# Kernel tuning notes

Hardware: AMD Instinct MI355X
Metric: run time of the kernel (lower is better)

## Reference

```python
import jax, jax.numpy as jnp
import numpy as np

HEADS = 8
DIM_HEAD = 64
SCALE = DIM_HEAD ** -0.5


def setup_inputs() -> dict:
    key = jax.random.key(0)
    ks = jax.random.split(key, 7)
    B, Nq, Nc = 4, 2048, 2048
    Dq, Dc = 1024, 768
    inner = HEADS * DIM_HEAD  # 512
    x = jax.random.normal(ks[0], (B, Nq, Dq), dtype=jnp.float32)
    context = jax.random.normal(ks[1], (B, Nc, Dc), dtype=jnp.float32)
    # Linear weights stored as (in, out) so y = x @ W, matching torch Linear math.
    Wq = jax.random.normal(ks[2], (Dq, inner), dtype=jnp.float32) * (Dq ** -0.5)
    Wk = jax.random.normal(ks[3], (Dc, inner), dtype=jnp.float32) * (Dc ** -0.5)
    Wv = jax.random.normal(ks[4], (Dc, inner), dtype=jnp.float32) * (Dc ** -0.5)
    Wo = jax.random.normal(ks[5], (inner, Dq), dtype=jnp.float32) * (inner ** -0.5)
    bo = jax.random.normal(ks[6], (Dq,), dtype=jnp.float32) * 0.01
    return {"x": x, "context": context, "Wq": Wq, "Wk": Wk, "Wv": Wv, "Wo": Wo, "bo": bo}


def reference(x, context, Wq, Wk, Wv, Wo, bo):
    B, Nq, _ = x.shape
    # projections -> [b, n, h, d]
    q = (x @ Wq).reshape(B, Nq, HEADS, DIM_HEAD)
    k = (context @ Wk).reshape(B, context.shape[1], HEADS, DIM_HEAD)
    v = (context @ Wv).reshape(B, context.shape[1], HEADS, DIM_HEAD)
    # scores [b, h, i, j]
    sim = jnp.einsum('bihd,bjhd->bhij', q, k) * SCALE
    attn = jax.nn.softmax(sim, axis=-1)
    out = jnp.einsum('bhij,bjhd->bihd', attn, v)  # [b, i, h, d]
    out = out.reshape(B, Nq, HEADS * DIM_HEAD)
    return out @ Wo + bo
```

## Files before the change

kernel.cpp:

```cpp
#include <hip/hip_runtime.h>
#include <hip/hip_bf16.h>


typedef __bf16 bf16_8 __attribute__((ext_vector_type(8)));
typedef __bf16 bf16_4 __attribute__((ext_vector_type(4)));
typedef float f32_4 __attribute__((ext_vector_type(4)));

#define AS1 __attribute__((address_space(1)))
#define AS3 __attribute__((address_space(3)))

__device__ __forceinline__ void gld_lds16(const __bf16* g, __bf16* l) {
  __builtin_amdgcn_global_load_lds((AS1 unsigned int*)(void*)g,
                                   (AS3 unsigned int*)(void*)l, 16, 0, 0);
}

__device__ __forceinline__ void lds_fence() {
  __asm__ volatile("" ::: "memory");
  __builtin_amdgcn_s_waitcnt(0xC07F);
  __asm__ volatile("" ::: "memory");
}

__global__ __launch_bounds__(256) void prep(
    const float* __restrict__ x, const float* __restrict__ ctx,
    const float* __restrict__ Wq, const float* __restrict__ Wk,
    const float* __restrict__ Wv, const float* __restrict__ Wo,
    __bf16* __restrict__ xb, __bf16* __restrict__ ctxb,
    __bf16* __restrict__ WqT, __bf16* __restrict__ WkT,
    __bf16* __restrict__ WvT, __bf16* __restrict__ WoT) {
  int tb = blockIdx.x;
  if (tb >= 1792) {
    tb -= 1792;
    const float* src;
    __bf16* dst;
    size_t base;
    if (tb < 4096) { src = x; dst = xb; base = (size_t)tb * 2048; }
    else { src = ctx; dst = ctxb; base = (size_t)(tb - 4096) * 2048; }
    const size_t idx = base + threadIdx.x * 8;
    const f32_4 f0 = *(const f32_4*)(src + idx);
    const f32_4 f1 = *(const f32_4*)(src + idx + 4);
    bf16_8 v;
#pragma unroll
    for (int i = 0; i < 4; ++i) { v[i] = (__bf16)f0[i]; v[4 + i] = (__bf16)f1[i]; }
    *(bf16_8*)(dst + idx) = v;
    return;
  }
  __shared__ __bf16 t[32][33];
  const float* W; __bf16* Wt; int K, N;
  if (tb < 512)       { W = Wq; Wt = WqT; K = 1024; N = 512; }
  else if (tb < 896)  { tb -= 512;  W = Wk; Wt = WkT; K = 768; N = 512; }
  else if (tb < 1280) { tb -= 896;  W = Wv; Wt = WvT; K = 768; N = 512; }
  else                { tb -= 1280; W = Wo; Wt = WoT; K = 512; N = 1024; }
  const int nx = N >> 5;
  const int n0 = (tb % nx) * 32, k0 = (tb / nx) * 32;
  const int tx = threadIdx.x & 31, ty = threadIdx.x >> 5;
#pragma unroll
  for (int r = 0; r < 32; r += 8)
    t[ty + r][tx] = (__bf16)W[(size_t)(k0 + ty + r) * N + n0 + tx];
  __syncthreads();
#pragma unroll
  for (int r = 0; r < 32; r += 8)
    Wt[(size_t)(n0 + ty + r) * K + k0 + tx] = t[tx][ty + r];
}

__global__ __launch_bounds__(256, 2) void proj(
    const __bf16* __restrict__ xb, const __bf16* __restrict__ ctxb,
    const __bf16* __restrict__ WqT, const __bf16* __restrict__ WkvT,
    __bf16* __restrict__ Qb, __bf16* __restrict__ Kbuf,
    __bf16* __restrict__ Vtb) {
  __shared__ __align__(16) __bf16 As[2][128 * 64];
  __shared__ __align__(16) __bf16 Bs[2][128 * 64];
  int tb = blockIdx.x;
  const __bf16 *A, *Bt;
  int K, bm, bn, mode;
  if (tb < 256) {
    A = xb; Bt = WqT; K = 1024; mode = 0;
    bn = (tb & 3) << 7; bm = (tb >> 2) << 7;
  } else {
    tb -= 256;
    A = ctxb; Bt = WkvT; K = 768; mode = 1;
    bn = (tb & 7) << 7; bm = (tb >> 3) << 7;
  }
  const int tid = threadIdx.x;
  const int lane = tid & 63;
  const int wave = tid >> 6;
  const int wi = (wave >> 1) * 64;
  const int wn = (wave & 1) * 64;
  const int lrow = lane & 15;
  const int quad = lane >> 4;
  const int lkey = lrow & 7;
  const int srow = tid >> 3;
  const int scol = (tid & 7) * 8;
  const int swz = (((scol >> 3) ^ (srow & 7)) * 8);

  f32_4 acc[4][4];
#pragma unroll
  for (int i = 0; i < 4; ++i)
#pragma unroll
    for (int j = 0; j < 4; ++j)
#pragma unroll
      for (int r = 0; r < 4; ++r) acc[i][j][r] = 0.0f;

  auto stage = [&](int buf, int kt) {
#pragma unroll
    for (int r = 0; r < 4; ++r) {
      const int row = r * 32 + srow;
      gld_lds16(A + (size_t)(bm + row) * K + kt + swz, &As[buf][row * 64 + scol]);
    }
#pragma unroll
    for (int r = 0; r < 4; ++r) {
      const int row = r * 32 + srow;
      gld_lds16(Bt + (size_t)(bn + row) * K + kt + swz, &Bs[buf][row * 64 + scol]);
    }
  };

  stage(0, 0);
  const int nkt = K >> 6;
  for (int kti = 0; kti < nkt; ++kti) {
    __syncthreads();
    if (kti + 1 < nkt) stage((kti + 1) & 1, (kti + 1) * 64);
    const __bf16* Asb = As[kti & 1];
    const __bf16* Bsb = Bs[kti & 1];
#pragma unroll
    for (int ks = 0; ks < 2; ++ks) {
      bf16_8 af[4], bfv[4];
#pragma unroll
      for (int t = 0; t < 4; ++t)
        af[t] = *(const bf16_8*)(Asb + (wi + t * 16 + lrow) * 64 +
                                 (((ks * 4 + quad) ^ lkey) * 8));
#pragma unroll
      for (int t = 0; t < 4; ++t)
        bfv[t] = *(const bf16_8*)(Bsb + (wn + t * 16 + lrow) * 64 +
                                  (((ks * 4 + quad) ^ lkey) * 8));
#pragma unroll
      for (int it = 0; it < 4; ++it)
#pragma unroll
        for (int nt = 0; nt < 4; ++nt)
          acc[it][nt] = __builtin_amdgcn_mfma_f32_16x16x32_bf16(
              af[it], bfv[nt], acc[it][nt], 0, 0, 0);
    }
  }

#pragma unroll
  for (int nt = 0; nt < 4; ++nt) {
    const int c = bn + wn + nt * 16 + lrow;
    if (mode == 0) {
#pragma unroll
      for (int it = 0; it < 4; ++it) {
        const int rbase = bm + wi + it * 16 + quad * 4;
#pragma unroll
        for (int r = 0; r < 4; ++r)
          Qb[(size_t)(rbase + r) * 512 + c] = (__bf16)(acc[it][nt][r] * 0.125f);
      }
    } else if (c < 512) {
#pragma unroll
      for (int it = 0; it < 4; ++it) {
        const int rbase = bm + wi + it * 16 + quad * 4;
#pragma unroll
        for (int r = 0; r < 4; ++r)
          Kbuf[(size_t)(rbase + r) * 512 + c] = (__bf16)acc[it][nt][r];
      }
    } else {
      const int vcol = c - 512;
      const int bhh = ((bm >> 11) << 3) + (vcol >> 6);
      const int d = vcol & 63;
#pragma unroll
      for (int it = 0; it < 4; ++it) {
        const int jb = (bm & 2047) + wi + it * 16 + quad * 4;
        bf16_4 pk;
#pragma unroll
        for (int r = 0; r < 4; ++r) pk[r] = (__bf16)acc[it][nt][r];
        *(bf16_4*)&Vtb[((size_t)(bhh * 64 + d)) * 2048 + jb] = pk;
      }
    }
  }
}

__global__ __launch_bounds__(256, 2) void attn_fwd(const __bf16* __restrict__ Q,
                                                   const __bf16* __restrict__ Kb,
                                                   const __bf16* __restrict__ Vt,
                                                   __bf16* __restrict__ AO) {
  __shared__ __align__(16) __bf16 Ks[2][64 * 64];
  __shared__ __align__(16) __bf16 Vs[2][64 * 64];
  __shared__ __align__(16) __bf16 Pl[4][32 * 64];
  const int tid = threadIdx.x;
  const int lane = tid & 63;
  const int wave = tid >> 6;
  const int bh = blockIdx.y;
  const int b = bh >> 3, h = bh & 7;
  const int i0 = blockIdx.x * 128 + wave * 32;
  const int lrow = lane & 15;
  const int quad = lane >> 4;
  const int lkey = lrow & 7;
  const size_t bq = (size_t)b * 2048;
  const int hc = h * 64;
  __bf16* Pw = &Pl[wave][0];

  const int ssub = lane >> 3;
  const int sch = lane & 7;
  const int sswz = (sch ^ ssub) * 8;

  const __bf16* Kg = Kb + bq * 512 + hc;
  const __bf16* Vg = Vt + (size_t)bh * 64 * 2048;

  auto stage = [&](int buf, int j0) {
#pragma unroll
    for (int t = 0; t < 2; ++t) {
      const int rb = wave * 16 + t * 8;
      gld_lds16(Kg + (size_t)(j0 + rb + ssub) * 512 + sswz, &Ks[buf][rb * 64]);
      gld_lds16(Vg + (size_t)(rb + ssub) * 2048 + j0 + sswz, &Vs[buf][rb * 64]);
    }
  };

  bf16_8 aq[2][2];
#pragma unroll
  for (int it = 0; it < 2; ++it)
#pragma unroll
    for (int ks = 0; ks < 2; ++ks)
      aq[it][ks] = *(const bf16_8*)(Q + (bq + i0 + it * 16 + lrow) * 512 +
                                    hc + ks * 32 + quad * 8);

  float psl[2] = {0.0f, 0.0f};
  f32_4 oacc[2][4];
#pragma unroll
  for (int it = 0; it < 2; ++it)
#pragma unroll
    for (int nt = 0; nt < 4; ++nt)
#pragma unroll
      for (int r = 0; r < 4; ++r) oacc[it][nt][r] = 0.0f;

  stage(0, 0);

  for (int jt = 0; jt < 32; ++jt) {
    __syncthreads();
    if (jt + 1 < 32) stage((jt + 1) & 1, (jt + 1) * 64);
    const __bf16* Ksb = Ks[jt & 1];
    const __bf16* Vsb = Vs[jt & 1];

    f32_4 sacc[2][4];
#pragma unroll
    for (int it = 0; it < 2; ++it)
#pragma unroll
      for (int jn = 0; jn < 4; ++jn)
#pragma unroll
        for (int r = 0; r < 4; ++r) sacc[it][jn][r] = 0.0f;
#pragma unroll
    for (int ks = 0; ks < 2; ++ks) {
      bf16_8 ak[4];
#pragma unroll
      for (int jn = 0; jn < 4; ++jn)
        ak[jn] = *(const bf16_8*)(Ksb + (jn * 16 + lrow) * 64 +
                                  (((ks * 4 + quad) ^ lkey) * 8));
#pragma unroll
      for (int it = 0; it < 2; ++it)
#pragma unroll
        for (int jn = 0; jn < 4; ++jn)
          sacc[it][jn] = __builtin_amdgcn_mfma_f32_16x16x32_bf16(
              ak[jn], aq[it][ks], sacc[it][jn], 0, 0, 0);
    }

#pragma unroll
    for (int it = 0; it < 2; ++it) {
      float ps = 0.0f;
#pragma unroll
      for (int jn = 0; jn < 4; ++jn) {
        bf16_4 pk;
#pragma unroll
        for (int r = 0; r < 4; ++r) {
          const float p = __expf(sacc[it][jn][r]);
          ps += p;
          pk[r] = (__bf16)p;
        }
        *(bf16_4*)(Pw + (it * 16 + lrow) * 64 +
                   (((2 * jn + (quad >> 1)) ^ lkey) * 8) + (quad & 1) * 4) = pk;
      }
      psl[it] += ps;
    }

    lds_fence();

#pragma unroll
    for (int ks2 = 0; ks2 < 2; ++ks2) {
      bf16_8 ap[2], bv[4];
#pragma unroll
      for (int it = 0; it < 2; ++it)
        ap[it] = *(const bf16_8*)(Pw + (it * 16 + lrow) * 64 +
                                  (((ks2 * 4 + quad) ^ lkey) * 8));
#pragma unroll
      for (int nt = 0; nt < 4; ++nt)
        bv[nt] = *(const bf16_8*)(Vsb + (nt * 16 + lrow) * 64 +
                                  (((ks2 * 4 + quad) ^ lkey) * 8));
#pragma unroll
      for (int it = 0; it < 2; ++it)
#pragma unroll
        for (int nt = 0; nt < 4; ++nt)
          oacc[it][nt] = __builtin_amdgcn_mfma_f32_16x16x32_bf16(
              ap[it], bv[nt], oacc[it][nt], 0, 0, 0);
    }
  }

#pragma unroll
  for (int it = 0; it < 2; ++it) {
    float ls = psl[it];
    ls += __shfl_xor(ls, 16);
    ls += __shfl_xor(ls, 32);
    const float inv = 1.0f / ls;
    float ic[4];
#pragma unroll
    for (int r = 0; r < 4; ++r) ic[r] = __shfl(inv, quad * 4 + r);
#pragma unroll
    for (int nt = 0; nt < 4; ++nt)
#pragma unroll
      for (int r = 0; r < 4; ++r) {
        const size_t rg = bq + i0 + it * 16 + quad * 4 + r;
        AO[rg * 512 + hc + nt * 16 + lrow] = (__bf16)(oacc[it][nt][r] * ic[r]);
      }
  }
}

__global__ __launch_bounds__(256, 2) void gemm_out(const __bf16* __restrict__ A,
                                                   const __bf16* __restrict__ Bt,
                                                   float* __restrict__ C,
                                                   const float* __restrict__ bias) {
  __shared__ __align__(16) __bf16 As[2][128 * 64];
  __shared__ __align__(16) __bf16 Bs[2][128 * 64];
  const int K = 512, N = 1024;
  const int tid = threadIdx.x;
  const int lane = tid & 63;
  const int wave = tid >> 6;
  const int wi = (wave >> 1) * 64;
  const int wn = (wave & 1) * 64;
  const int bm = blockIdx.y * 128;
  const int bn = blockIdx.x * 128;
  const int lrow = lane & 15;
  const int quad = lane >> 4;
  const int lkey = lrow & 7;
  const int srow = tid >> 3;
  const int scol = (tid & 7) * 8;
  const int swz = (((scol >> 3) ^ (srow & 7)) * 8);

  f32_4 acc[4][4];
#pragma unroll
  for (int i = 0; i < 4; ++i)
#pragma unroll
    for (int j = 0; j < 4; ++j)
#pragma unroll
      for (int r = 0; r < 4; ++r) acc[i][j][r] = 0.0f;

  auto stage = [&](int buf, int kt) {
#pragma unroll
    for (int r = 0; r < 4; ++r) {
      const int row = r * 32 + srow;
      gld_lds16(A + (size_t)(bm + row) * K + kt + swz, &As[buf][row * 64 + scol]);
      gld_lds16(Bt + (size_t)(bn + row) * K + kt + swz, &Bs[buf][row * 64 + scol]);
    }
  };

  stage(0, 0);
  for (int kti = 0; kti < 8; ++kti) {
    __syncthreads();
    if (kti + 1 < 8) stage((kti + 1) & 1, (kti + 1) * 64);
    const __bf16* Asb = As[kti & 1];
    const __bf16* Bsb = Bs[kti & 1];
#pragma unroll
    for (int ks = 0; ks < 2; ++ks) {
      bf16_8 af[4], bfv[4];
#pragma unroll
      for (int t = 0; t < 4; ++t)
        af[t] = *(const bf16_8*)(Asb + (wi + t * 16 + lrow) * 64 +
                                 (((ks * 4 + quad) ^ lkey) * 8));
#pragma unroll
      for (int t = 0; t < 4; ++t)
        bfv[t] = *(const bf16_8*)(Bsb + (wn + t * 16 + lrow) * 64 +
                                  (((ks * 4 + quad) ^ lkey) * 8));
#pragma unroll
      for (int it = 0; it < 4; ++it)
#pragma unroll
        for (int nt = 0; nt < 4; ++nt)
          acc[it][nt] = __builtin_amdgcn_mfma_f32_16x16x32_bf16(
              af[it], bfv[nt], acc[it][nt], 0, 0, 0);
    }
  }

#pragma unroll
  for (int nt = 0; nt < 4; ++nt) {
    const int c = bn + wn + nt * 16 + lrow;
    const float bv = bias[c];
#pragma unroll
    for (int it = 0; it < 4; ++it) {
      const int rbase = bm + wi + it * 16 + quad * 4;
#pragma unroll
      for (int r = 0; r < 4; ++r)
        C[(size_t)(rbase + r) * N + c] = acc[it][nt][r] + bv;
    }
  }
}

extern "C" void kernel_launch(void* const* d_in, const int* in_sizes, int n_in,
                              void* d_out, int out_size, void* d_ws, size_t ws_size,
                              hipStream_t stream) {
  (void)in_sizes; (void)n_in; (void)out_size; (void)ws_size;
  const float* x   = (const float*)d_in[0];
  const float* ctx = (const float*)d_in[1];
  const float* Wq  = (const float*)d_in[2];
  const float* Wk  = (const float*)d_in[3];
  const float* Wv  = (const float*)d_in[4];
  const float* Wo  = (const float*)d_in[5];
  const float* bo  = (const float*)d_in[6];

  __bf16* ws = (__bf16*)d_ws;
  __bf16* WqT  = ws;
  __bf16* WkT  = WqT + 512 * 1024;
  __bf16* WvT  = WkT + 512 * 768;
  __bf16* WoT  = WvT + 512 * 768;
  __bf16* Qb   = WoT + 1024 * 512;
  __bf16* Kbuf = Qb + 8192 * 512;
  __bf16* Vtb  = Kbuf + 8192 * 512;
  __bf16* AOb  = Vtb + 8192 * 512;
  __bf16* xb   = AOb + 8192 * 512;
  __bf16* ctxb = xb + 8192 * 1024;

  prep<<<8960, 256, 0, stream>>>(x, ctx, Wq, Wk, Wv, Wo,
                                 xb, ctxb, WqT, WkT, WvT, WoT);

  proj<<<768, 256, 0, stream>>>(xb, ctxb, WqT, WkT, Qb, Kbuf, Vtb);

  attn_fwd<<<dim3(16, 32), 256, 0, stream>>>(Qb, Kbuf, Vtb, AOb);

  gemm_out<<<dim3(8, 64), 256, 0, stream>>>(AOb, WoT, (float*)d_out, bo);
}
```

Measured before the change: 220.0 us.

## Shrink attention tile to 16 rows per wave, raise occupancy, add XCD-aware block mapping

```diff
diff --git a/kernel.cpp b/kernel.cpp
--- a/kernel.cpp
+++ b/kernel.cpp
@@ -175,19 +175,22 @@
   }
 }
 
-__global__ __launch_bounds__(256, 2) void attn_fwd(const __bf16* __restrict__ Q,
+__global__ __launch_bounds__(256, 4) void attn_fwd(const __bf16* __restrict__ Q,
                                                    const __bf16* __restrict__ Kb,
                                                    const __bf16* __restrict__ Vt,
                                                    __bf16* __restrict__ AO) {
   __shared__ __align__(16) __bf16 Ks[2][64 * 64];
   __shared__ __align__(16) __bf16 Vs[2][64 * 64];
-  __shared__ __align__(16) __bf16 Pl[4][32 * 64];
+  __shared__ __align__(16) __bf16 Pl[4][16 * 64];
   const int tid = threadIdx.x;
   const int lane = tid & 63;
   const int wave = tid >> 6;
-  const int bh = blockIdx.y;
+  const int did = blockIdx.x;
+  const int sid = did >> 3;
+  const int bh = ((did & 7) << 2) + (sid & 3);
+  const int ib = sid >> 2;
   const int b = bh >> 3, h = bh & 7;
-  const int i0 = blockIdx.x * 128 + wave * 32;
+  const int i0 = ib * 64 + wave * 16;
   const int lrow = lane & 15;
   const int quad = lane >> 4;
   const int lkey = lrow & 7;
@@ -211,22 +214,18 @@
     }
   };
 
-  bf16_8 aq[2][2];
-#pragma unroll
-  for (int it = 0; it < 2; ++it)
-#pragma unroll
-    for (int ks = 0; ks < 2; ++ks)
-      aq[it][ks] = *(const bf16_8*)(Q + (bq + i0 + it * 16 + lrow) * 512 +
-                                    hc + ks * 32 + quad * 8);
-
-  float psl[2] = {0.0f, 0.0f};
-  f32_4 oacc[2][4];
-#pragma unroll
-  for (int it = 0; it < 2; ++it)
-#pragma unroll
-    for (int nt = 0; nt < 4; ++nt)
-#pragma unroll
-      for (int r = 0; r < 4; ++r) oacc[it][nt][r] = 0.0f;
+  bf16_8 aq[2];
+#pragma unroll
+  for (int ks = 0; ks < 2; ++ks)
+    aq[ks] = *(const bf16_8*)(Q + (bq + i0 + lrow) * 512 +
+                              hc + ks * 32 + quad * 8);
+
+  float psl = 0.0f;
+  f32_4 oacc[4];
+#pragma unroll
+  for (int nt = 0; nt < 4; ++nt)
+#pragma unroll
+    for (int r = 0; r < 4; ++r) oacc[nt][r] = 0.0f;
 
   stage(0, 0);
 
@@ -236,13 +235,12 @@
     const __bf16* Ksb = Ks[jt & 1];
     const __bf16* Vsb = Vs[jt & 1];
 
-    f32_4 sacc[2][4];
-#pragma unroll
-    for (int it = 0; it < 2; ++it)
-#pragma unroll
-      for (int jn = 0; jn < 4; ++jn)
-#pragma unroll
-        for (int r = 0; r < 4; ++r) sacc[it][jn][r] = 0.0f;
+    f32_4 sacc[4];
+#pragma unroll
+    for (int jn = 0; jn < 4; ++jn)
+#pragma unroll
+      for (int r = 0; r < 4; ++r) sacc[jn][r] = 0.0f;
+    __builtin_amdgcn_s_setprio(1);
 #pragma unroll
     for (int ks = 0; ks < 2; ++ks) {
       bf16_8 ak[4];
@@ -251,56 +249,50 @@
         ak[jn] = *(const bf16_8*)(Ksb + (jn * 16 + lrow) * 64 +
                                   (((ks * 4 + quad) ^ lkey) * 8));
 #pragma unroll
-      for (int it = 0; it < 2; ++it)
-#pragma unroll
-        for (int jn = 0; jn < 4; ++jn)
-          sacc[it][jn] = __builtin_amdgcn_mfma_f32_16x16x32_bf16(
-              ak[jn], aq[it][ks], sacc[it][jn], 0, 0, 0);
-    }
-
-#pragma unroll
-    for (int it = 0; it < 2; ++it) {
+      for (int jn = 0; jn < 4; ++jn)
+        sacc[jn] = __builtin_amdgcn_mfma_f32_16x16x32_bf16(
+            ak[jn], aq[ks], sacc[jn], 0, 0, 0);
+    }
+    __builtin_amdgcn_s_setprio(0);
+
+    {
       float ps = 0.0f;
 #pragma unroll
       for (int jn = 0; jn < 4; ++jn) {
         bf16_4 pk;
 #pragma unroll
         for (int r = 0; r < 4; ++r) {
-          const float p = __expf(sacc[it][jn][r]);
+          const float p = __expf(sacc[jn][r]);
           ps += p;
           pk[r] = (__bf16)p;
         }
-        *(bf16_4*)(Pw + (it * 16 + lrow) * 64 +
+        *(bf16_4*)(Pw + lrow * 64 +
                    (((2 * jn + (quad >> 1)) ^ lkey) * 8) + (quad & 1) * 4) = pk;
       }
-      psl[it] += ps;
+      psl += ps;
     }
 
     lds_fence();
 
+    __builtin_amdgcn_s_setprio(1);
 #pragma unroll
     for (int ks2 = 0; ks2 < 2; ++ks2) {
-      bf16_8 ap[2], bv[4];
-#pragma unroll
-      for (int it = 0; it < 2; ++it)
-        ap[it] = *(const bf16_8*)(Pw + (it * 16 + lrow) * 64 +
-                                  (((ks2 * 4 + quad) ^ lkey) * 8));
+      bf16_8 ap, bv[4];
+      ap = *(const bf16_8*)(Pw + lrow * 64 + (((ks2 * 4 + quad) ^ lkey) * 8));
 #pragma unroll
       for (int nt = 0; nt < 4; ++nt)
         bv[nt] = *(const bf16_8*)(Vsb + (nt * 16 + lrow) * 64 +
                                   (((ks2 * 4 + quad) ^ lkey) * 8));
 #pragma unroll
-      for (int it = 0; it < 2; ++it)
-#pragma unroll
-        for (int nt = 0; nt < 4; ++nt)
-          oacc[it][nt] = __builtin_amdgcn_mfma_f32_16x16x32_bf16(
-              ap[it], bv[nt], oacc[it][nt], 0, 0, 0);
-    }
-  }
-
-#pragma unroll
-  for (int it = 0; it < 2; ++it) {
-    float ls = psl[it];
+      for (int nt = 0; nt < 4; ++nt)
+        oacc[nt] = __builtin_amdgcn_mfma_f32_16x16x32_bf16(
+            ap, bv[nt], oacc[nt], 0, 0, 0);
+    }
+    __builtin_amdgcn_s_setprio(0);
+  }
+
+  {
+    float ls = psl;
     ls += __shfl_xor(ls, 16);
     ls += __shfl_xor(ls, 32);
     const float inv = 1.0f / ls;
@@ -311,8 +303,8 @@
     for (int nt = 0; nt < 4; ++nt)
 #pragma unroll
       for (int r = 0; r < 4; ++r) {
-        const size_t rg = bq + i0 + it * 16 + quad * 4 + r;
-        AO[rg * 512 + hc + nt * 16 + lrow] = (__bf16)(oacc[it][nt][r] * ic[r]);
+        const size_t rg = bq + i0 + quad * 4 + r;
+        AO[rg * 512 + hc + nt * 16 + lrow] = (__bf16)(oacc[nt][r] * ic[r]);
       }
   }
 }
@@ -424,7 +416,7 @@
 
   proj<<<768, 256, 0, stream>>>(xb, ctxb, WqT, WkT, Qb, Kbuf, Vtb);
 
-  attn_fwd<<<dim3(16, 32), 256, 0, stream>>>(Qb, Kbuf, Vtb, AOb);
+  attn_fwd<<<1024, 256, 0, stream>>>(Qb, Kbuf, Vtb, AOb);
 
   gemm_out<<<dim3(8, 64), 256, 0, stream>>>(AOb, WoT, (float*)d_out, bo);
 }
```

Result: no change. 221.1 us (+0.5%).
